# Optimization experiments

Measured on AMD Instinct MI355X. Metric: run time of the kernel, lower is better.

The kernel has to match this reference:

```python
import jax, jax.numpy as jnp
import numpy as np

T, B, H, W, F = 128, 1, 32, 32, 512
HID, HH, WW = 128, 32, 32


def setup_inputs() -> dict:
    key = jax.random.key(0)
    kx, kh, kwx, kwh = jax.random.split(key, 4)
    x = jax.random.normal(kx, (T, B, H, W, F), dtype=jnp.float32)
    h = jax.random.normal(kh, (B, HID, HH, WW), dtype=jnp.float32)
    Wx = jax.random.normal(kwx, (1, F), dtype=jnp.float32) * (1.0 / np.sqrt(F))
    Wh = jax.random.normal(kwh, (1, HID), dtype=jnp.float32) * (1.0 / np.sqrt(HID))
    return {"x": x, "h": h, "Wx": Wx, "Wh": Wh}


def reference(x, h, Wx, Wh):
    # Per-timestep mean-pool over spatial dims of x[i] ([B,H,W,F] -> [B,F]),
    # batched over all T timesteps at once (replaces the python loop).
    pooled_x = jnp.mean(x, axis=(2, 3))              # [T, B, F]
    att_x = jnp.einsum('tbf,of->tbo', pooled_x, Wx)  # [T, B, 1]
    # Hidden state mean-pool over spatial dims ([B,HID,HH,WW] -> [B,HID]).
    pooled_h = jnp.mean(h, axis=(2, 3))              # [B, HID]
    att_h = jnp.einsum('bd,od->bo', pooled_h, Wh)    # [B, 1]
    e = (att_x + att_h)[:, :, 0]                     # [T, B]
    e = jnp.squeeze(e)                               # [T] (B == 1, mimics np .squeeze())
    weights = jax.nn.softmax(e, axis=0)              # softmax over time steps
    return weights[:, None, None, None]              # [T, 1, 1, 1]
```

## Files before the change

### kernel.cpp

```cpp
#include <hip/hip_runtime.h>


#define T_STEPS 128
#define HW      1024
#define F4      128
#define BPT     16
#define THREADS 256
#define F4_PER_BLOCK (HW * F4 / BPT)
#define ITERS   (F4_PER_BLOCK / THREADS)

__global__ __launch_bounds__(THREADS) void ta_dot_kernel(
    const float4* __restrict__ x, const float* __restrict__ Wx,
    float* __restrict__ partial)
{
    const int tid = threadIdx.x;
    const int t   = blockIdx.x / BPT;
    const int b   = blockIdx.x % BPT;

    const float4 w = reinterpret_cast<const float4*>(Wx)[tid & (F4 - 1)];

    const float4* xt = x + (size_t)t * (HW * F4) + b * F4_PER_BLOCK + tid;

    float acc = 0.0f;
#pragma unroll
    for (int i = 0; i < ITERS; ++i) {
        float4 v = xt[(size_t)i * THREADS];
        acc = fmaf(v.x, w.x, acc);
        acc = fmaf(v.y, w.y, acc);
        acc = fmaf(v.z, w.z, acc);
        acc = fmaf(v.w, w.w, acc);
    }

    for (int o = 32; o > 0; o >>= 1) acc += __shfl_xor(acc, o);

    __shared__ float s[THREADS / 64];
    if ((tid & 63) == 0) s[tid >> 6] = acc;
    __syncthreads();
    if (tid == 0) partial[blockIdx.x] = s[0] + s[1] + s[2] + s[3];
}

__global__ __launch_bounds__(T_STEPS) void ta_softmax_kernel(
    const float* __restrict__ partial, float* __restrict__ out)
{
    const int tid = threadIdx.x;

    float e = 0.0f;
#pragma unroll
    for (int i = 0; i < BPT; ++i) e += partial[tid * BPT + i];
    e *= (1.0f / (float)HW);

    float m = e;
    for (int o = 32; o > 0; o >>= 1) m = fmaxf(m, __shfl_xor(m, o));

    __shared__ float smax[2], ssum[2];
    const int wave = tid >> 6;
    if ((tid & 63) == 0) smax[wave] = m;
    __syncthreads();
    const float gm = fmaxf(smax[0], smax[1]);

    const float ex = expf(e - gm);
    float s = ex;
    for (int o = 32; o > 0; o >>= 1) s += __shfl_xor(s, o);
    if ((tid & 63) == 0) ssum[wave] = s;
    __syncthreads();

    out[tid] = ex / (ssum[0] + ssum[1]);
}

extern "C" void kernel_launch(void* const* d_in, const int* in_sizes, int n_in,
                              void* d_out, int out_size, void* d_ws, size_t ws_size,
                              hipStream_t stream) {
    const float* x  = (const float*)d_in[0];
    const float* Wx = (const float*)d_in[2];

    float* partial = (float*)d_ws;
    float* out     = (float*)d_out;

    ta_dot_kernel<<<T_STEPS * BPT, THREADS, 0, stream>>>(
        (const float4*)x, Wx, partial);
    ta_softmax_kernel<<<1, T_STEPS, 0, stream>>>(partial, out);
}
```

Baseline: 46.08 us.

## Fuse softmax into dot kernel via last-block atomic counter

Merges the reduction and softmax kernels into one launch. Each block writes its partial sum, fences, and bumps a global atomic counter, and the last block to arrive performs the final reduction and softmax. This removes the second kernel launch and its gap, but adds a hipMemsetAsync on the counter each call plus atomics and fences. The __syncthreads calls inside the tid<T_STEPS branch are divergent across waves, though the block is made of whole waves.

```diff
diff --git a/kernel.cpp b/kernel.cpp
--- a/kernel.cpp
+++ b/kernel.cpp
@@ -6,12 +6,14 @@
 #define F4      128
 #define BPT     16
 #define THREADS 256
+#define NBLOCKS (T_STEPS * BPT)
 #define F4_PER_BLOCK (HW * F4 / BPT)
 #define ITERS   (F4_PER_BLOCK / THREADS)
 
-__global__ __launch_bounds__(THREADS) void ta_dot_kernel(
+__global__ __launch_bounds__(THREADS) void ta_fused_kernel(
     const float4* __restrict__ x, const float* __restrict__ Wx,
-    float* __restrict__ partial)
+    float* __restrict__ partial, unsigned int* __restrict__ counter,
+    float* __restrict__ out)
 {
     const int tid = threadIdx.x;
     const int t   = blockIdx.x / BPT;
@@ -34,37 +36,44 @@
     for (int o = 32; o > 0; o >>= 1) acc += __shfl_xor(acc, o);
 
     __shared__ float s[THREADS / 64];
+    __shared__ unsigned int s_old;
     if ((tid & 63) == 0) s[tid >> 6] = acc;
     __syncthreads();
-    if (tid == 0) partial[blockIdx.x] = s[0] + s[1] + s[2] + s[3];
-}
 
-__global__ __launch_bounds__(T_STEPS) void ta_softmax_kernel(
-    const float* __restrict__ partial, float* __restrict__ out)
-{
-    const int tid = threadIdx.x;
+    if (tid == 0) {
+        partial[blockIdx.x] = s[0] + s[1] + s[2] + s[3];
+        __threadfence();
+        s_old = atomicAdd(counter, 1u);
+    }
+    __syncthreads();
+    if (s_old != NBLOCKS - 1) return;
 
-    float e = 0.0f;
+    __threadfence();
+    __shared__ float smax[2], ssum[2];
+
+    if (tid < T_STEPS) {
+        float e = 0.0f;
 #pragma unroll
-    for (int i = 0; i < BPT; ++i) e += partial[tid * BPT + i];
-    e *= (1.0f / (float)HW);
+        for (int i = 0; i < BPT; ++i)
+            e += __hip_atomic_load(&partial[tid * BPT + i],
+                                   __ATOMIC_ACQUIRE, __HIP_MEMORY_SCOPE_AGENT);
+        e *= (1.0f / (float)HW);
 
-    float m = e;
-    for (int o = 32; o > 0; o >>= 1) m = fmaxf(m, __shfl_xor(m, o));
+        float m = e;
+        for (int o = 32; o > 0; o >>= 1) m = fmaxf(m, __shfl_xor(m, o));
+        const int wave = tid >> 6;
+        if ((tid & 63) == 0) smax[wave] = m;
+        __syncthreads();
+        const float gm = fmaxf(smax[0], smax[1]);
 
-    __shared__ float smax[2], ssum[2];
-    const int wave = tid >> 6;
-    if ((tid & 63) == 0) smax[wave] = m;
-    __syncthreads();
-    const float gm = fmaxf(smax[0], smax[1]);
+        const float ex = expf(e - gm);
+        float sm = ex;
+        for (int o = 32; o > 0; o >>= 1) sm += __shfl_xor(sm, o);
+        if ((tid & 63) == 0) ssum[wave] = sm;
+        __syncthreads();
 
-    const float ex = expf(e - gm);
-    float s = ex;
-    for (int o = 32; o > 0; o >>= 1) s += __shfl_xor(s, o);
-    if ((tid & 63) == 0) ssum[wave] = s;
-    __syncthreads();
-
-    out[tid] = ex / (ssum[0] + ssum[1]);
+        out[tid] = ex / (ssum[0] + ssum[1]);
+    }
 }
 
 extern "C" void kernel_launch(void* const* d_in, const int* in_sizes, int n_in,
@@ -73,10 +82,12 @@
     const float* x  = (const float*)d_in[0];
     const float* Wx = (const float*)d_in[2];
 
-    float* partial = (float*)d_ws;
-    float* out     = (float*)d_out;
+    float*        partial = (float*)d_ws;
+    unsigned int* counter = (unsigned int*)((char*)d_ws + NBLOCKS * sizeof(float));
+    float*        out     = (float*)d_out;
 
-    ta_dot_kernel<<<T_STEPS * BPT, THREADS, 0, stream>>>(
-        (const float4*)x, Wx, partial);
-    ta_softmax_kernel<<<1, T_STEPS, 0, stream>>>(partial, out);
+    hipMemsetAsync(counter, 0, sizeof(unsigned int), stream);
+
+    ta_fused_kernel<<<NBLOCKS, THREADS, 0, stream>>>(
+        (const float4*)x, Wx, partial, counter, out);
 }
```

Result: slower. 115.0 us (+149.6%).
